# Optimization experiments

Measured on AMD Instinct MI355X. Metric: run time of the kernel, lower is better.

## Reference

```python
import jax, jax.numpy as jnp
import numpy as np

B, T, E, H = 4, 2048, 1024, 16
S = E // H  # 64


def setup_inputs() -> dict:
    key = jax.random.key(0)
    ks = jax.random.split(key, 6)
    return {
        "x": jax.random.normal(ks[0], (B, T, E), dtype=jnp.float32),
        "Wk": jax.random.normal(ks[1], (S, S), dtype=jnp.float32) * (1.0 / np.sqrt(S)),
        "Wq": jax.random.normal(ks[2], (S, S), dtype=jnp.float32) * (1.0 / np.sqrt(S)),
        "Wv": jax.random.normal(ks[3], (S, S), dtype=jnp.float32) * (1.0 / np.sqrt(S)),
        "Wp": jax.random.normal(ks[4], (E, E), dtype=jnp.float32) * (1.0 / np.sqrt(E)),
        "bp": jnp.zeros((E,), dtype=jnp.float32),
    }


def reference(x, Wk, Wq, Wv, Wp, bp):
    b, t, e = x.shape
    h, s = H, S
    xh = x.reshape(b, t, h, s)
    # per-head projections share one (s,s) weight across all heads (torch Linear: y = x @ W.T)
    keys = jnp.einsum('bthi,oi->bhto', xh, Wk)     # (b,h,t,s)
    queries = jnp.einsum('bthi,oi->bhto', xh, Wq)
    values = jnp.einsum('bthi,oi->bhto', xh, Wv)
    scale = e ** 0.25  # q and k each divided by e^(1/4) -> net 1/sqrt(e)
    queries = queries / scale
    keys = keys / scale
    dot = jnp.einsum('bhqs,bhks->bhqk', queries, keys)  # (b,h,t,t)
    attn = jax.nn.softmax(dot, axis=-1)
    out = jnp.einsum('bhqk,bhks->bqhs', attn, values)   # (b,t,h,s)
    out = out.reshape(b, t, h * s)
    return jnp.einsum('bte,oe->bto', out, Wp) + bp
```

## Files before the change

kernel.cpp:

```cpp
#include <hip/hip_runtime.h>
#include <hip/hip_bf16.h>

#define Bv 4
#define Tv 2048
#define Ev 1024
#define Hv 16
#define Sv 64

typedef __attribute__((ext_vector_type(8))) short bf16x8;
typedef __attribute__((ext_vector_type(4))) short bf16x4;
typedef __attribute__((ext_vector_type(4))) float f32x4;
typedef __attribute__((ext_vector_type(16))) float f32x16;

__device__ __forceinline__ ushort f2bf(float f) {
    unsigned u = __float_as_uint(f);
    u = (u + 0x7FFFu + ((u >> 16) & 1u)) >> 16;
    return (ushort)u;
}
__device__ __forceinline__ unsigned pkrn(float a, float b) {
    __hip_bfloat162 t = __float22bfloat162_rn(make_float2(a, b));
    unsigned r; __builtin_memcpy(&r, &t, 4); return r;
}
__device__ __forceinline__ unsigned pktr(float a, float b) {
    return __builtin_amdgcn_perm(__float_as_uint(b), __float_as_uint(a), 0x07060302u);
}

__device__ __forceinline__ void async16(void* lds, const void* g) {
    __builtin_amdgcn_global_load_lds(
        (const __attribute__((address_space(1))) unsigned int*)g,
        (__attribute__((address_space(3))) unsigned int*)lds, 16, 0, 0);
}

__global__ __launch_bounds__(256) void cast_kernel(
    const float* __restrict__ Wp, const float* __restrict__ Wq,
    const float* __restrict__ Wk, const float* __restrict__ Wv,
    ushort* __restrict__ Wpb, ushort* __restrict__ Wqb,
    ushort* __restrict__ Wkb, ushort* __restrict__ Wvb)
{
    int blk = blockIdx.x;
    if (blk < 1024) {
        int i = (blk * 256 + threadIdx.x) * 4;
        float4 v = *(const float4*)(Wp + i);
        uint2 o = {pkrn(v.x, v.y), pkrn(v.z, v.w)};
        *(uint2*)(Wpb + i) = o;
    } else {
        int p = blk - 1024;
        const float* src = (p == 0) ? Wq : ((p == 1) ? Wk : Wv);
        ushort* dst      = (p == 0) ? Wqb : ((p == 1) ? Wkb : Wvb);
        const float scale = (p == 0) ? 0.03125f * 1.4426950408889634f : 1.0f;
        #pragma unroll
        for (int it = 0; it < 4; ++it) {
            int i = (it * 256 + threadIdx.x) * 4;
            float4 v = *(const float4*)(src + i);
            uint2 o = {pkrn(v.x * scale, v.y * scale), pkrn(v.z * scale, v.w * scale)};
            *(uint2*)(dst + i) = o;
        }
    }
}

__global__ __launch_bounds__(192) void qkv_kernel(
    const float* __restrict__ x,
    const ushort* __restrict__ Wqb, const ushort* __restrict__ Wkb,
    const ushort* __restrict__ Wvb,
    ushort* __restrict__ Q, ushort* __restrict__ K, ushort* __restrict__ Vt)
{
    const int tid  = threadIdx.x;
    const int wave = tid >> 6;
    const int lane = tid & 63;
    const int m    = lane & 15;
    const int quad = lane >> 4;

    const ushort* Wsel = (wave == 0) ? Wqb : ((wave == 1) ? Wkb : Wvb);
    bf16x8 wf[4][2];
    #pragma unroll
    for (int ot = 0; ot < 4; ++ot)
        #pragma unroll
        for (int ks = 0; ks < 2; ++ks)
            wf[ot][ks] = *(const bf16x8*)&Wsel[(ot * 16 + m) * 64 + ks * 32 + quad * 8];

    const int tt = blockIdx.x >> 2;
    const int hg = blockIdx.x & 3;
    const int g0 = tt * 16;
    const int gm = g0 + m;
    const int b  = g0 >> 11;
    const int t0 = g0 & 2047;

    #pragma unroll
    for (int hi = 0; hi < 4; ++hi) {
        const int h  = hg * 4 + hi;
        const int bh = b * Hv + h;

        bf16x8 xf[2];
        #pragma unroll
        for (int ks = 0; ks < 2; ++ks) {
            const float* src = x + (size_t)gm * Ev + h * Sv + ks * 32 + quad * 8;
            float4 v0 = *(const float4*)src;
            float4 v1 = *(const float4*)(src + 4);
            unsigned pk[4];
            pk[0] = pkrn(v0.x, v0.y); pk[1] = pkrn(v0.z, v0.w);
            pk[2] = pkrn(v1.x, v1.y); pk[3] = pkrn(v1.z, v1.w);
            xf[ks] = *(bf16x8*)pk;
        }

        f32x4 acc[4];
        #pragma unroll
        for (int ot = 0; ot < 4; ++ot) acc[ot] = (f32x4){0.f, 0.f, 0.f, 0.f};

        if (wave < 2) {
            #pragma unroll
            for (int ks = 0; ks < 2; ++ks)
                #pragma unroll
                for (int ot = 0; ot < 4; ++ot)
                    acc[ot] = __builtin_amdgcn_mfma_f32_16x16x32_bf16(
                        wf[ot][ks], xf[ks], acc[ot], 0, 0, 0);
            ushort* dst = ((wave == 0) ? Q : K)
                        + ((size_t)bh * Tv + t0 + m) * Sv + quad * 4;
            #pragma unroll
            for (int ot = 0; ot < 4; ++ot) {
                uint2 w = {pkrn(acc[ot][0], acc[ot][1]), pkrn(acc[ot][2], acc[ot][3])};
                *(uint2*)(dst + ot * 16) = w;
            }
        } else {
            #pragma unroll
            for (int ks = 0; ks < 2; ++ks)
                #pragma unroll
                for (int st = 0; st < 4; ++st)
                    acc[st] = __builtin_amdgcn_mfma_f32_16x16x32_bf16(
                        xf[ks], wf[st][ks], acc[st], 0, 0, 0);
            ushort* vr = Vt + ((size_t)bh * Sv + m) * Tv + t0 + quad * 4;
            #pragma unroll
            for (int st = 0; st < 4; ++st) {
                uint2 w = {pkrn(acc[st][0], acc[st][1]), pkrn(acc[st][2], acc[st][3])};
                *(uint2*)(vr + (size_t)st * 16 * Tv) = w;
            }
        }
    }
}

__global__ __launch_bounds__(256, 2) void attn_kernel(
    const ushort* __restrict__ Q, const ushort* __restrict__ K,
    const ushort* __restrict__ Vt, ushort* __restrict__ O)
{
    __shared__ ushort kl[64 * 64];
    __shared__ ushort vl[64 * 64];
    __shared__ float  ll[4][64];

    const int tid  = threadIdx.x;
    const int wave = tid >> 6;
    const int lane = tid & 63;
    const int r31  = lane & 31;
    const int hi   = lane >> 5;
    const int bh   = blockIdx.x & 63;
    const int q0   = (blockIdx.x >> 6) << 8;

    const ushort* Qb = Q + ((size_t)bh * Tv + q0 + wave * 64 + r31) * Sv + hi * 8;
    bf16x8 qf[2][4];
    #pragma unroll
    for (int g = 0; g < 2; ++g)
        #pragma unroll
        for (int ks = 0; ks < 4; ++ks)
            qf[g][ks] = *(const bf16x8*)(Qb + (size_t)g * 32 * Sv + ks * 16);

    f32x16 oa[2][2];
    #pragma unroll
    for (int g = 0; g < 2; ++g)
        #pragma unroll
        for (int st = 0; st < 2; ++st)
            #pragma unroll
            for (int r = 0; r < 16; ++r)
                oa[g][st][r] = 0.f;
    float lsum[2] = {0.f, 0.f};

    const ushort* Kb = K  + (size_t)bh * Tv * Sv;
    const ushort* Vb = Vt + (size_t)bh * Sv * Tv;

    const int r0 = tid >> 3,         cg0 = (tid & 7) ^ (r0 & 7);
    const int r1 = (256 + tid) >> 3, cg1 = ((256 + tid) & 7) ^ (r1 & 7);
    const size_t koff0 = (size_t)r0 * Sv + cg0 * 8;
    const size_t koff1 = (size_t)r1 * Sv + cg1 * 8;
    const size_t voff0 = (size_t)r0 * Tv + cg0 * 8;
    const size_t voff1 = (size_t)r1 * Tv + cg1 * 8;
    const int swz = r31 & 7;

    auto softpv = [&](const f32x16& sv, float& ls, f32x16* oag, int kp,
                      const bf16x8* vf) {
        float p[8];
        #pragma unroll
        for (int j = 0; j < 8; ++j)
            p[j] = __builtin_amdgcn_exp2f(sv[kp * 8 + j]);
        ls += ((p[0] + p[1]) + (p[2] + p[3]))
            + ((p[4] + p[5]) + (p[6] + p[7]));
        unsigned d0 = pktr(p[0], p[1]);
        unsigned d1 = pktr(p[2], p[3]);
        unsigned d2 = pktr(p[4], p[5]);
        unsigned d3 = pktr(p[6], p[7]);
        asm volatile("v_permlane32_swap_b32 %0, %1" : "+v"(d0), "+v"(d2));
        asm volatile("v_permlane32_swap_b32 %0, %1" : "+v"(d1), "+v"(d3));
        unsigned pw[4] = {d0, d1, d2, d3};
        bf16x8 pf = *(bf16x8*)pw;
        #pragma unroll
        for (int st = 0; st < 2; ++st)
            oag[st] = __builtin_amdgcn_mfma_f32_32x32x16_bf16(
                pf, vf[st], oag[st], 0, 0, 0);
    };

    for (int k0 = 0; k0 < Tv; k0 += 64) {
        __syncthreads();
        async16(&kl[(size_t)tid * 8],         Kb + (size_t)k0 * Sv + koff0);
        async16(&kl[((size_t)tid + 256) * 8], Kb + (size_t)k0 * Sv + koff1);
        async16(&vl[(size_t)tid * 8],         Vb + k0 + voff0);
        async16(&vl[((size_t)tid + 256) * 8], Vb + k0 + voff1);
        __syncthreads();

        #pragma unroll
        for (int kt = 0; kt < 2; ++kt) {
            bf16x8 kf[4];
            #pragma unroll
            for (int ks = 0; ks < 4; ++ks)
                kf[ks] = *(const bf16x8*)
                    &kl[(kt * 32 + r31) * 64 + (((ks * 2 + hi) ^ swz) * 8)];

            f32x16 s0, s1;
            #pragma unroll
            for (int r = 0; r < 16; ++r) { s0[r] = 0.f; s1[r] = 0.f; }
            #pragma unroll
            for (int ks = 0; ks < 4; ++ks)
                s0 = __builtin_amdgcn_mfma_f32_32x32x16_bf16(
                    kf[ks], qf[0][ks], s0, 0, 0, 0);
            #pragma unroll
            for (int ks = 0; ks < 4; ++ks)
                s1 = __builtin_amdgcn_mfma_f32_32x32x16_bf16(
                    kf[ks], qf[1][ks], s1, 0, 0, 0);

            #pragma unroll
            for (int kp = 0; kp < 2; ++kp) {
                const int kc = (kt * 2 + kp) * 2 + hi;
                bf16x8 vf[2];
                #pragma unroll
                for (int st = 0; st < 2; ++st)
                    vf[st] = *(const bf16x8*)
                        &vl[(st * 32 + r31) * 64 + ((kc ^ swz) * 8)];
                softpv(s0, lsum[0], oa[0], kp, vf);
                softpv(s1, lsum[1], oa[1], kp, vf);
            }
        }
    }

    lsum[0] += __shfl_xor(lsum[0], 32, 64);
    lsum[1] += __shfl_xor(lsum[1], 32, 64);
    if (hi == 0) {
        ll[wave][r31]      = 1.0f / lsum[0];
        ll[wave][32 + r31] = 1.0f / lsum[1];
    }

    const int b = bh >> 4, h = bh & 15;
    #pragma unroll
    for (int g = 0; g < 2; ++g) {
        float sc[16];
        #pragma unroll
        for (int r = 0; r < 16; ++r)
            sc[r] = ll[wave][g * 32 + (r & 3) + 4 * hi + 8 * (r >> 2)];
        #pragma unroll
        for (int st = 0; st < 2; ++st)
            #pragma unroll
            for (int r = 0; r < 16; ++r) {
                const int q = (r & 3) + 4 * hi + 8 * (r >> 2);
                O[((size_t)(b * Tv + q0 + wave * 64 + g * 32 + q)) * Ev
                  + h * Sv + st * 32 + r31] = f2bf(oa[g][st][r] * sc[r]);
            }
    }
}

__global__ __launch_bounds__(256) void proj_kernel(
    const ushort* __restrict__ A, const ushort* __restrict__ B,
    const float* __restrict__ bp, float* __restrict__ C)
{
    __shared__ ushort Asm[128 * 32];
    __shared__ ushort Bsm[128 * 32];
    const int tid  = threadIdx.x;
    const int wave = tid >> 6;
    const int lane = tid & 63;
    const int m    = lane & 15;
    const int quad = lane >> 4;
    const int wm   = wave >> 1;
    const int wn   = wave & 1;
    const int m0   = blockIdx.x * 128;
    const int n0   = blockIdx.y * 128;

    f32x4 acc[4][4];
    #pragma unroll
    for (int i = 0; i < 4; ++i)
        #pragma unroll
        for (int j = 0; j < 4; ++j)
            acc[i][j] = (f32x4){0.f, 0.f, 0.f, 0.f};

    for (int k0 = 0; k0 < Ev; k0 += 32) {
        __syncthreads();
        #pragma unroll
        for (int j = 0; j < 2; ++j) {
            int c   = j * 256 + tid;
            int row = c >> 2;
            int col = (c & 3) * 8;
            async16(&Asm[c * 8], &A[(size_t)(m0 + row) * Ev + k0 + col]);
            async16(&Bsm[c * 8], &B[(size_t)(n0 + row) * Ev + k0 + col]);
        }
        __syncthreads();

        bf16x8 af[4], bf[4];
        #pragma unroll
        for (int i = 0; i < 4; ++i)
            af[i] = *(const bf16x8*)&Asm[(wm * 64 + i * 16 + m) * 32 + quad * 8];
        #pragma unroll
        for (int j = 0; j < 4; ++j)
            bf[j] = *(const bf16x8*)&Bsm[(wn * 64 + j * 16 + m) * 32 + quad * 8];
        #pragma unroll
        for (int i = 0; i < 4; ++i)
            #pragma unroll
            for (int j = 0; j < 4; ++j)
                acc[i][j] = __builtin_amdgcn_mfma_f32_16x16x32_bf16(
                    af[i], bf[j], acc[i][j], 0, 0, 0);
    }

    float bbv[4];
    #pragma unroll
    for (int j = 0; j < 4; ++j)
        bbv[j] = bp[n0 + wn * 64 + j * 16 + m];

    #pragma unroll
    for (int i = 0; i < 4; ++i)
        #pragma unroll
        for (int j = 0; j < 4; ++j)
            #pragma unroll
            for (int r = 0; r < 4; ++r)
                C[(size_t)(m0 + wm * 64 + i * 16 + quad * 4 + r) * Ev
                  + n0 + wn * 64 + j * 16 + m] = acc[i][j][r] + bbv[j];
}

extern "C" void kernel_launch(void* const* d_in, const int* in_sizes, int n_in,
                              void* d_out, int out_size, void* d_ws, size_t ws_size,
                              hipStream_t stream) {
    const float* x  = (const float*)d_in[0];
    const float* Wk = (const float*)d_in[1];
    const float* Wq = (const float*)d_in[2];
    const float* Wv = (const float*)d_in[3];
    const float* Wp = (const float*)d_in[4];
    const float* bp = (const float*)d_in[5];
    float* out = (float*)d_out;

    ushort* Q   = (ushort*)d_ws;
    ushort* K   = Q   + 8388608;
    ushort* Vt  = K   + 8388608;
    ushort* O   = Vt  + 8388608;
    ushort* Wpb = O   + 8388608;
    ushort* Wqb = Wpb + 1048576;
    ushort* Wkb = Wqb + 4096;
    ushort* Wvb = Wkb + 4096;

    cast_kernel<<<1027, 256, 0, stream>>>(Wp, Wq, Wk, Wv, Wpb, Wqb, Wkb, Wvb);
    qkv_kernel<<<2048, 192, 0, stream>>>(x, Wqb, Wkb, Wvb, Q, K, Vt);
    attn_kernel<<<512, 256, 0, stream>>>(Q, K, Vt, O);
    proj_kernel<<<dim3(64, 8), 256, 0, stream>>>(O, Wpb, bp, out);
}
```

Baseline: 218.2 us.

## Double-buffer K/V tiles in LDS with register prefetch in attention loop

Replaces the synchronous async-copy load of each K/V tile (two barriers per iteration) with double-buffered LDS and a register-staged prefetch two tiles ahead. Each iteration writes the prefetched tile into the other buffer, issues global loads for the next tile, then computes on the current buffer, ending with a single barrier. This is meant to hide global-load latency behind MFMA work and drop one barrier per iteration. In exchange it doubles LDS use for K/V and adds 16 VGPRs for staging, which could pressure occupancy at launch bounds (256, 2).

```diff
diff --git a/kernel.cpp b/kernel.cpp
--- a/kernel.cpp
+++ b/kernel.cpp
@@ -141,8 +141,8 @@
     const ushort* __restrict__ Q, const ushort* __restrict__ K,
     const ushort* __restrict__ Vt, ushort* __restrict__ O)
 {
-    __shared__ ushort kl[64 * 64];
-    __shared__ ushort vl[64 * 64];
+    __shared__ ushort kl[2][64 * 64];
+    __shared__ ushort vl[2][64 * 64];
     __shared__ float  ll[4][64];
 
     const int tid  = threadIdx.x;
@@ -204,13 +204,33 @@
                 pf, vf[st], oag[st], 0, 0, 0);
     };
 
+    uint4 rk0 = *(const uint4*)(Kb + koff0);
+    uint4 rk1 = *(const uint4*)(Kb + koff1);
+    uint4 rv0 = *(const uint4*)(Vb + voff0);
+    uint4 rv1 = *(const uint4*)(Vb + voff1);
+    *(uint4*)&kl[0][(size_t)tid * 8]         = rk0;
+    *(uint4*)&kl[0][((size_t)tid + 256) * 8] = rk1;
+    *(uint4*)&vl[0][(size_t)tid * 8]         = rv0;
+    *(uint4*)&vl[0][((size_t)tid + 256) * 8] = rv1;
+    rk0 = *(const uint4*)(Kb + (size_t)64 * Sv + koff0);
+    rk1 = *(const uint4*)(Kb + (size_t)64 * Sv + koff1);
+    rv0 = *(const uint4*)(Vb + 64 + voff0);
+    rv1 = *(const uint4*)(Vb + 64 + voff1);
+    __syncthreads();
+
     for (int k0 = 0; k0 < Tv; k0 += 64) {
-        __syncthreads();
-        async16(&kl[(size_t)tid * 8],         Kb + (size_t)k0 * Sv + koff0);
-        async16(&kl[((size_t)tid + 256) * 8], Kb + (size_t)k0 * Sv + koff1);
-        async16(&vl[(size_t)tid * 8],         Vb + k0 + voff0);
-        async16(&vl[((size_t)tid + 256) * 8], Vb + k0 + voff1);
-        __syncthreads();
+        const int cur = (k0 >> 6) & 1;
+
+        *(uint4*)&kl[cur ^ 1][(size_t)tid * 8]         = rk0;
+        *(uint4*)&kl[cur ^ 1][((size_t)tid + 256) * 8] = rk1;
+        *(uint4*)&vl[cur ^ 1][(size_t)tid * 8]         = rv0;
+        *(uint4*)&vl[cur ^ 1][((size_t)tid + 256) * 8] = rv1;
+
+        int kn = k0 + 128; if (kn >= Tv) kn = 0;
+        rk0 = *(const uint4*)(Kb + (size_t)kn * Sv + koff0);
+        rk1 = *(const uint4*)(Kb + (size_t)kn * Sv + koff1);
+        rv0 = *(const uint4*)(Vb + kn + voff0);
+        rv1 = *(const uint4*)(Vb + kn + voff1);
 
         #pragma unroll
         for (int kt = 0; kt < 2; ++kt) {
@@ -218,7 +238,7 @@
             #pragma unroll
             for (int ks = 0; ks < 4; ++ks)
                 kf[ks] = *(const bf16x8*)
-                    &kl[(kt * 32 + r31) * 64 + (((ks * 2 + hi) ^ swz) * 8)];
+                    &kl[cur][(kt * 32 + r31) * 64 + (((ks * 2 + hi) ^ swz) * 8)];
 
             f32x16 s0, s1;
             #pragma unroll
@@ -239,11 +259,13 @@
                 #pragma unroll
                 for (int st = 0; st < 2; ++st)
                     vf[st] = *(const bf16x8*)
-                        &vl[(st * 32 + r31) * 64 + ((kc ^ swz) * 8)];
+                        &vl[cur][(st * 32 + r31) * 64 + ((kc ^ swz) * 8)];
                 softpv(s0, lsum[0], oa[0], kp, vf);
                 softpv(s1, lsum[1], oa[1], kp, vf);
             }
         }
+
+        __syncthreads();
     }
 
     lsum[0] += __shfl_xor(lsum[0], 32, 64);
```

After: 220.4 us. About the same (+1.0%).
